# Optimization experiments

Measured on AMD Instinct MI355X. Metric: run time of the kernel, lower is better.

Reference implementation:

```python
import jax, jax.numpy as jnp
import numpy as np

B, T, C = 4, 2048, 1024
H, D, CS = 16, 64, 16   # heads, head dim, titans chunk size
EPS = 1e-5


def setup_inputs():
    key = jax.random.key(0)
    ks = jax.random.split(key, 4)
    s = 0.02
    return {
        "x": jax.random.normal(ks[0], (B, T, C), jnp.float32),
        "W_attn": jax.random.normal(ks[1], (C, 3 * C), jnp.float32) * s,
        "b_attn": jnp.zeros((3 * C,), jnp.float32),
        "W_param": jax.random.normal(ks[2], (C, 3 * H), jnp.float32) * s,
        "b_param": jnp.zeros((3 * H,), jnp.float32),
        "W_proj": jax.random.normal(ks[3], (C, C), jnp.float32) * s,
        "b_proj": jnp.zeros((C,), jnp.float32),
        "w": jnp.ones((H, D), jnp.float32),
        "b": jnp.zeros((H, D), jnp.float32),
    }


def _ln(x, w, b):
    # per-head layernorm over last dim
    mu = x.mean(-1, keepdims=True)
    xc = x - mu
    rstd = jax.lax.rsqrt((xc * xc).mean(-1, keepdims=True) + EPS)
    return xc * rstd * w + b


def _ln_bwd(x, w, dy):
    # gradient of layernorm(x; w, b) w.r.t. x, given upstream dy
    mu = x.mean(-1, keepdims=True)
    xc = x - mu
    rstd = jax.lax.rsqrt((xc * xc).mean(-1, keepdims=True) + EPS)
    xhat = xc * rstd
    wdy = dy * w
    c1 = (xhat * wdy).mean(-1, keepdims=True)
    c2 = wdy.mean(-1, keepdims=True)
    return (wdy - xhat * c1 - c2) * rstd


def _chunk_titans_linear(q, k, v, w, b, theta, alpha, eta):
    # q,k,v: [B,H,T,D]; theta/alpha/eta: [B,H,T,1]; w,b: [H,D]
    NT = T // CS
    wr = w.reshape(1, H, 1, D)
    br = b.reshape(1, H, 1, D)

    def to_chunks(t):
        return t.reshape(B, H, NT, CS, t.shape[-1]).transpose(2, 0, 1, 3, 4)

    qc, kc, vc = to_chunks(q), to_chunks(k), to_chunks(v)
    tc, ac, ec = to_chunks(theta), to_chunks(alpha), to_chunks(eta)

    def chunk_step(carry, inp):
        S, m = carry  # memory state / momentum: [B,H,D,D]
        q_i, k_i, v_i, th_i, al_i, et_i = inp
        # gradients of ||LN(k S) - v||^2 w.r.t. S, taken at the chunk-start state
        kh = jnp.einsum('bhcd,bhde->bhce', k_i, S)
        d_recon = 2.0 * (_ln(kh, wr, br) - v_i)
        dkh = _ln_bwd(kh, wr, d_recon)
        grads = jnp.einsum('bhci,bhcj->bhcij', k_i, dkh)  # [B,H,CS,D,D]

        def tok_step(c2, t_inp):
            S_t, m_t = c2
            g, th, al, et = t_inp
            th = th[..., None]; al = al[..., None]; et = et[..., None]
            m_t = et * m_t - th * g          # momentum
            S_t = (1.0 - al) * S_t + m_t     # weight-decayed state update
            return (S_t, m_t), S_t

        (S, m), S_seq = jax.lax.scan(
            tok_step, (S, m),
            (grads.transpose(2, 0, 1, 3, 4),
             th_i.transpose(2, 0, 1, 3),
             al_i.transpose(2, 0, 1, 3),
             et_i.transpose(2, 0, 1, 3)))
        # read memory with the freshly updated per-token state
        o_i = jnp.einsum('bhcd,cbhde->bhce', q_i, S_seq)
        return (S, m), o_i

    S0 = jnp.zeros((B, H, D, D), q.dtype)
    m0 = jnp.zeros((B, H, D, D), q.dtype)
    _, o_chunks = jax.lax.scan(chunk_step, (S0, m0), (qc, kc, vc, tc, ac, ec))
    o = o_chunks.transpose(1, 2, 0, 3, 4).reshape(B, H, T, D)
    return _ln(o, wr, br)  # normalized memory readout


def reference(x, W_attn, b_attn, W_param, b_param, W_proj, b_proj, w, b):
    qkv = x @ W_attn + b_attn
    q, k, v = jnp.split(qkv, 3, axis=-1)

    def heads(t):
        return t.reshape(B, T, H, D).transpose(0, 2, 1, 3)

    q, k, v = heads(q), heads(k), heads(v)
    q = q / jnp.maximum(jnp.linalg.norm(q, axis=-1, keepdims=True), 1e-12)
    k = k / jnp.maximum(jnp.linalg.norm(k, axis=-1, keepdims=True), 1e-12)
    p = jax.nn.sigmoid((x @ W_param + b_param).reshape(B, T, H, 3).transpose(0, 2, 1, 3))
    theta, alpha, eta = p[..., 0:1], p[..., 1:2], p[..., 2:3]
    o = _chunk_titans_linear(q, k, v, w, b, theta, alpha, eta)
    o = o.transpose(0, 2, 1, 3).reshape(B, T, C)
    return o @ W_proj + b_proj
```

## Files before the change

kernel.cpp:

```cpp
#include <hip/hip_runtime.h>
#include <cstddef>
#include <cstdint>
#include <math.h>

#define BB   4
#define TT   2048
#define CCH  1024
#define HH   16
#define DD   64
#define CSZ  16
#define NTC  128
#define EPSF 1e-5f
#define WVS  8
#define STR  3072

typedef __attribute__((ext_vector_type(8))) short bf16x8;
typedef __attribute__((ext_vector_type(4))) float f32x4;
typedef __attribute__((ext_vector_type(2))) float f32x2;

__device__ __forceinline__ void bar_lds() {
  asm volatile("s_waitcnt lgkmcnt(0)" ::: "memory");
  __builtin_amdgcn_s_barrier();
}

__device__ __forceinline__ uint32_t pack_split(float f) {
  uint32_t b = __float_as_uint(f);
  uint32_t uh = (b + 0x7fffu + ((b >> 16) & 1u)) >> 16;
  float fh = __uint_as_float(uh << 16);
  float r = f - fh;
  return uh | (__float_as_uint(r) & 0xffff0000u);
}
__device__ __forceinline__ float unpack_f(uint32_t u) {
  return __uint_as_float(u << 16) + __uint_as_float(u & 0xffff0000u);
}

__device__ __forceinline__ float wave_sum(float x) {
  float v = x;
  v += __int_as_float(__builtin_amdgcn_update_dpp(0, __float_as_int(v), 0x111, 0xf, 0xf, true));
  v += __int_as_float(__builtin_amdgcn_update_dpp(0, __float_as_int(v), 0x112, 0xf, 0xf, true));
  v += __int_as_float(__builtin_amdgcn_update_dpp(0, __float_as_int(v), 0x114, 0xf, 0xf, true));
  v += __int_as_float(__builtin_amdgcn_update_dpp(0, __float_as_int(v), 0x118, 0xf, 0xf, true));
  v += __int_as_float(__builtin_amdgcn_update_dpp(0, __float_as_int(v), 0x142, 0xa, 0xf, true));
  v += __int_as_float(__builtin_amdgcn_update_dpp(0, __float_as_int(v), 0x143, 0xc, 0xf, true));
  return __int_as_float(__builtin_amdgcn_readlane(__float_as_int(v), 63));
}

__device__ __forceinline__ float red16(float x) {
  float v = x;
  v += __int_as_float(__builtin_amdgcn_update_dpp(0, __float_as_int(v), 0x0B1, 0xf, 0xf, true));
  v += __int_as_float(__builtin_amdgcn_update_dpp(0, __float_as_int(v), 0x04E, 0xf, 0xf, true));
  v += __int_as_float(__builtin_amdgcn_update_dpp(0, __float_as_int(v), 0x124, 0xf, 0xf, true));
  v += __int_as_float(__builtin_amdgcn_update_dpp(0, __float_as_int(v), 0x128, 0xf, 0xf, true));
  return v;
}

__device__ __forceinline__ float sigmoidf_(float x) {
  return 1.f / (1.f + expf(-x));
}

__global__ __launch_bounds__(256) void split_transpose_pl(
    const float* __restrict__ W, unsigned short* __restrict__ Whi,
    unsigned short* __restrict__ Wlo, int K, int N, int rowOff) {
  __shared__ float t[32][33];
  const int n0 = blockIdx.x * 32, k0 = blockIdx.y * 32;
  const int tx = threadIdx.x & 31, ty = threadIdx.x >> 5;
#pragma unroll
  for (int i = 0; i < 4; i++) {
    int n = n0 + tx;
    t[ty + i * 8][tx] = (n < N) ? W[(size_t)(k0 + ty + i * 8) * N + n] : 0.f;
  }
  __syncthreads();
#pragma unroll
  for (int i = 0; i < 4; i++) {
    int n = n0 + ty + i * 8;
    if (n < N) {
      uint32_t ps = pack_split(t[tx][ty + i * 8]);
      size_t off = (size_t)(rowOff + n) * K + k0 + tx;
      Whi[off] = (unsigned short)(ps & 0xffffu);
      Wlo[off] = (unsigned short)(ps >> 16);
    }
  }
}

template<bool A_PACKED, bool C_PACKED, bool NORM>
__global__ __launch_bounds__(256) void gemm_split(
    const void* __restrict__ Av, int lda,
    const unsigned short* __restrict__ Bhg,
    const unsigned short* __restrict__ Blg,
    const float* __restrict__ bias,
    void* __restrict__ Cv, float* __restrict__ Pbuf,
    int M, int ldc, int K, int Nb, int Ns, int pc0) {
  __shared__ unsigned short Ahi[128][40];
  __shared__ unsigned short Alo[128][40];
  __shared__ unsigned short Bhi[128][40];
  __shared__ unsigned short Blo[128][40];

  const int tid = threadIdx.x;
  const int row0 = blockIdx.y * 128;
  const int col0 = blockIdx.x * 128;
  const int wv = tid >> 6;
  const int l  = tid & 63;
  const int wr = wv >> 1, wc = wv & 1;
  const int lrow = l & 15;
  const int kgrp = (l >> 4) * 8;

  const int sr = tid >> 1;
  const int sk = (tid & 1) * 16;

  f32x4 acc[4][4];
#pragma unroll
  for (int i = 0; i < 4; i++)
#pragma unroll
    for (int j = 0; j < 4; j++) acc[i][j] = (f32x4){0.f, 0.f, 0.f, 0.f};

  uint4 pa[4];
  float4 pf[4];
  uint4 pbh[2], pbl[2];

  auto load_tile = [&](int k0) {
    if (A_PACKED) {
      const uint32_t* Ap = (const uint32_t*)Av + (size_t)(row0 + sr) * lda + k0 + sk;
#pragma unroll
      for (int i = 0; i < 4; i++) pa[i] = *(const uint4*)(Ap + i * 4);
    } else {
      const float* Ap = (const float*)Av + (size_t)(row0 + sr) * lda + k0 + sk;
#pragma unroll
      for (int i = 0; i < 4; i++) pf[i] = *(const float4*)(Ap + i * 4);
    }
    if (col0 + sr < Nb) {
      const unsigned short* bh = Bhg + (size_t)(col0 + sr) * K + k0 + sk;
      const unsigned short* bl = Blg + (size_t)(col0 + sr) * K + k0 + sk;
      pbh[0] = *(const uint4*)bh;  pbh[1] = *(const uint4*)(bh + 8);
      pbl[0] = *(const uint4*)bl;  pbl[1] = *(const uint4*)(bl + 8);
    } else {
      pbh[0] = pbh[1] = pbl[0] = pbl[1] = make_uint4(0u, 0u, 0u, 0u);
    }
  };

  auto commit_tile = [&]() {
    uint32_t hp[8], lp[8];
    if (A_PACKED) {
      uint32_t u[16];
#pragma unroll
      for (int i = 0; i < 4; i++) *(uint4*)&u[i * 4] = pa[i];
#pragma unroll
      for (int j = 0; j < 8; j++) {
        hp[j] = (u[2 * j] & 0xffffu) | (u[2 * j + 1] << 16);
        lp[j] = (u[2 * j] >> 16) | (u[2 * j + 1] & 0xffff0000u);
      }
    } else {
      float f[16];
#pragma unroll
      for (int i = 0; i < 4; i++) *(float4*)&f[i * 4] = pf[i];
      uint32_t uh[16], ulr[16];
#pragma unroll
      for (int j = 0; j < 16; j++) {
        uint32_t b = __float_as_uint(f[j]);
        uint32_t h = (b + 0x7fffu + ((b >> 16) & 1u)) >> 16;
        uh[j] = h;
        ulr[j] = __float_as_uint(f[j] - __uint_as_float(h << 16));
      }
#pragma unroll
      for (int j = 0; j < 8; j++) {
        hp[j] = uh[2 * j] | (uh[2 * j + 1] << 16);
        lp[j] = (ulr[2 * j] >> 16) | (ulr[2 * j + 1] & 0xffff0000u);
      }
    }
    *(uint4*)&Ahi[sr][sk]     = *(uint4*)&hp[0];
    *(uint4*)&Ahi[sr][sk + 8] = *(uint4*)&hp[4];
    *(uint4*)&Alo[sr][sk]     = *(uint4*)&lp[0];
    *(uint4*)&Alo[sr][sk + 8] = *(uint4*)&lp[4];
    *(uint4*)&Bhi[sr][sk]     = pbh[0];
    *(uint4*)&Bhi[sr][sk + 8] = pbh[1];
    *(uint4*)&Blo[sr][sk]     = pbl[0];
    *(uint4*)&Blo[sr][sk + 8] = pbl[1];
  };

  load_tile(0);
  for (int k0 = 0; k0 < K; k0 += 32) {
    commit_tile();
    bar_lds();
    if (k0 + 32 < K) load_tile(k0 + 32);

    bf16x8 bh[4], bl[4];
#pragma unroll
    for (int j = 0; j < 4; j++) {
      bh[j] = *(const bf16x8*)&Bhi[wc * 64 + j * 16 + lrow][kgrp];
      bl[j] = *(const bf16x8*)&Blo[wc * 64 + j * 16 + lrow][kgrp];
    }
#pragma unroll
    for (int i = 0; i < 4; i++) {
      bf16x8 ah = *(const bf16x8*)&Ahi[wr * 64 + i * 16 + lrow][kgrp];
      bf16x8 al = *(const bf16x8*)&Alo[wr * 64 + i * 16 + lrow][kgrp];
#pragma unroll
      for (int j = 0; j < 4; j++) {
        acc[i][j] = __builtin_amdgcn_mfma_f32_16x16x32_bf16(ah, bh[j], acc[i][j], 0, 0, 0);
        acc[i][j] = __builtin_amdgcn_mfma_f32_16x16x32_bf16(ah, bl[j], acc[i][j], 0, 0, 0);
        acc[i][j] = __builtin_amdgcn_mfma_f32_16x16x32_bf16(al, bh[j], acc[i][j], 0, 0, 0);
      }
    }
    bar_lds();
  }

  const int crow4 = (l >> 4) * 4;
  if (NORM && col0 < 2048) {
    float bj[4];
#pragma unroll
    for (int j = 0; j < 4; j++) bj[j] = bias[col0 + wc * 64 + j * 16 + lrow];
#pragma unroll
    for (int i = 0; i < 4; i++) {
#pragma unroll
      for (int r = 0; r < 4; r++) {
        float vals[4];
        float ss = 0.f;
#pragma unroll
        for (int j = 0; j < 4; j++) {
          vals[j] = acc[i][j][r] + bj[j];
          ss += vals[j] * vals[j];
        }
        ss = red16(ss);
        float sc = 1.f / fmaxf(sqrtf(ss), 1e-12f);
        const int rowb = row0 + wr * 64 + i * 16 + crow4 + r;
#pragma unroll
        for (int j = 0; j < 4; j++) {
          const int col = col0 + wc * 64 + j * 16 + lrow;
          ((uint32_t*)Cv)[(size_t)rowb * ldc + col] = pack_split(vals[j] * sc);
        }
      }
    }
  } else {
#pragma unroll
    for (int i = 0; i < 4; i++) {
#pragma unroll
      for (int j = 0; j < 4; j++) {
        const int col = col0 + wc * 64 + j * 16 + lrow;
        const float bv = (col < Ns) ? bias[col] : 0.f;
        const int rowb = row0 + wr * 64 + i * 16 + crow4;
#pragma unroll
        for (int r = 0; r < 4; r++) {
          float v = acc[i][j][r] + bv;
          if (col < Ns) {
            if (col >= pc0) {
              Pbuf[(size_t)(rowb + r) * 48 + (col - pc0)] = v;
            } else if (C_PACKED) {
              ((uint32_t*)Cv)[(size_t)(rowb + r) * ldc + col] = pack_split(v);
            } else {
              ((float*)Cv)[(size_t)(rowb + r) * ldc + col] = v;
            }
          }
        }
      }
    }
  }
}

__global__ __launch_bounds__(512) void titans_rec(
    uint32_t* __restrict__ qkv, const float* __restrict__ p,
    const float* __restrict__ w, const float* __restrict__ bparm) {
  const int bh = blockIdx.x;
  const int b = bh >> 4;
  const int h = bh & 15;
  const int tid = threadIdx.x;
  const int wv = tid >> 6;
  const int l = tid & 63;

  __shared__ float k_s[2][CSZ][DD];
  __shared__ float q_s[2][CSZ][DD];
  __shared__ float v_s[CSZ][DD];
  __shared__ float dkh_s[CSZ][DD];
  __shared__ float part[2][WVS][CSZ][DD];
  __shared__ float4 prm_s[2][CSZ];

  f32x2 S2[4], M2[4];
#pragma unroll
  for (int r = 0; r < 4; r++) { S2[r] = (f32x2){0.f, 0.f}; M2[r] = (f32x2){0.f, 0.f}; }

  const float w_l = w[h * DD + l];
  const float b_l = bparm[h * DD + l];

  uint32_t* qbase = qkv + (size_t)(b * TT) * STR + h * DD;
  const float* pbase = p + (size_t)(b * TT) * 48 + h * 3;

  uint32_t rq[2], rk[2], rv[2];
  float rp0 = 0.f, rp1 = 0.f, rp2 = 0.f;
  {
#pragma unroll
    for (int i = 0; i < 2; i++) {
      const int row = wv + i * 8;
      size_t roff = (size_t)row * STR + l;
      q_s[0][row][l] = unpack_f(qbase[roff]);
      k_s[0][row][l] = unpack_f(qbase[roff + 1024]);
      v_s[row][l]    = unpack_f(qbase[roff + 2048]);
    }
    if (tid < CSZ) {
      const float* pp = pbase + (size_t)tid * 48;
      prm_s[0][tid] = make_float4(sigmoidf_(pp[0]), sigmoidf_(pp[1]), sigmoidf_(pp[2]), 0.f);
    }
#pragma unroll
    for (int i = 0; i < 2; i++) {
      size_t roff = (size_t)(CSZ + wv + i * 8) * STR + l;
      rq[i] = qbase[roff];
      rk[i] = qbase[roff + 1024];
      rv[i] = qbase[roff + 2048];
    }
    if (tid < CSZ) {
      const float* pp = pbase + (size_t)(CSZ + tid) * 48;
      rp0 = pp[0]; rp1 = pp[1]; rp2 = pp[2];
    }
  }
  bar_lds();

  for (int nt = 0; nt < NTC; nt++) {
    const int buf = nt & 1;
    float (*partw)[CSZ][DD] = part[buf];
    float (*partr)[CSZ][DD] = part[buf ^ 1];

    if (nt > 0) {
#pragma unroll
      for (int i = 0; i < 2; i++) {
        const int t = wv + i * 8;
        float o = 0.f;
#pragma unroll
        for (int ww = 0; ww < WVS; ww++) o += partr[ww][t][l];
        float mu = wave_sum(o) * (1.f / 64.f);
        float xc = o - mu;
        float var = wave_sum(xc * xc) * (1.f / 64.f);
        float rstd = rsqrtf(var + EPSF);
        float y = xc * rstd * w_l + b_l;
        qbase[(size_t)((nt - 1) * CSZ + t) * STR + 2048 + l] = pack_split(y);
      }
    }
#pragma unroll
    for (int c = 0; c < CSZ; c++) {
      const f32x2* kp2 = (const f32x2*)&k_s[buf][c][wv * 8];
      f32x2 a2;
      a2 = kp2[0] * S2[0];
      a2 = kp2[1] * S2[1] + a2;
      a2 = kp2[2] * S2[2] + a2;
      a2 = kp2[3] * S2[3] + a2;
      partw[wv][c][l] = a2.x + a2.y;
    }
    bar_lds();

#pragma unroll
    for (int i = 0; i < 2; i++) {
      const int c = wv + i * 8;
      float kh = 0.f;
#pragma unroll
      for (int ww = 0; ww < WVS; ww++) kh += partw[ww][c][l];
      float mu = wave_sum(kh) * (1.f / 64.f);
      float xc = kh - mu;
      float var = wave_sum(xc * xc) * (1.f / 64.f);
      float rstd = rsqrtf(var + EPSF);
      float xhat = xc * rstd;
      float y = xhat * w_l + b_l;
      float dy = 2.f * (y - v_s[c][l]);
      float wdy = dy * w_l;
      float c1 = wave_sum(xhat * wdy) * (1.f / 64.f);
      float c2 = wave_sum(wdy) * (1.f / 64.f);
      dkh_s[c][l] = (wdy - xhat * c1 - c2) * rstd;
    }
    bar_lds();

    if (nt + 1 < NTC) {
#pragma unroll
      for (int i = 0; i < 2; i++) {
        const int row = wv + i * 8;
        k_s[buf ^ 1][row][l] = unpack_f(rk[i]);
        q_s[buf ^ 1][row][l] = unpack_f(rq[i]);
        v_s[row][l] = unpack_f(rv[i]);
      }
      if (tid < CSZ)
        prm_s[buf ^ 1][tid] = make_float4(sigmoidf_(rp0), sigmoidf_(rp1), sigmoidf_(rp2), 0.f);
    }
    if (nt + 2 < NTC) {
#pragma unroll
      for (int i = 0; i < 2; i++) {
        size_t roff = (size_t)((nt + 2) * CSZ + wv + i * 8) * STR + l;
        rq[i] = qbase[roff];
        rk[i] = qbase[roff + 1024];
        rv[i] = qbase[roff + 2048];
      }
      if (tid < CSZ) {
        const float* pp = pbase + (size_t)((nt + 2) * CSZ + tid) * 48;
        rp0 = pp[0]; rp1 = pp[1]; rp2 = pp[2];
      }
    }
#pragma unroll
    for (int t = 0; t < CSZ; t++) {
      float4 prm = prm_s[buf][t];
      float a = prm.x * dkh_s[t][l];
      const f32x2 na2 = (f32x2){-a, -a};
      const f32x2 et2 = (f32x2){prm.z, prm.z};
      const f32x2 be2 = (f32x2){1.f - prm.y, 1.f - prm.y};
      const f32x2* kp2 = (const f32x2*)&k_s[buf][t][wv * 8];
      const f32x2* qp2 = (const f32x2*)&q_s[buf][t][wv * 8];
      f32x2 po2 = (f32x2){0.f, 0.f};
#pragma unroll
      for (int pq = 0; pq < 4; pq++) {
        M2[pq] = et2 * M2[pq] + na2 * kp2[pq];
        S2[pq] = be2 * S2[pq] + M2[pq];
        po2    = qp2[pq] * S2[pq] + po2;
      }
      partw[wv][t][l] = po2.x + po2.y;
    }
    bar_lds();
  }

  {
    float (*partr)[CSZ][DD] = part[(NTC - 1) & 1];
#pragma unroll
    for (int i = 0; i < 2; i++) {
      const int t = wv + i * 8;
      float o = 0.f;
#pragma unroll
      for (int ww = 0; ww < WVS; ww++) o += partr[ww][t][l];
      float mu = wave_sum(o) * (1.f / 64.f);
      float xc = o - mu;
      float var = wave_sum(xc * xc) * (1.f / 64.f);
      float rstd = rsqrtf(var + EPSF);
      float y = xc * rstd * w_l + b_l;
      qbase[(size_t)((NTC - 1) * CSZ + t) * STR + 2048 + l] = pack_split(y);
    }
  }
}

extern "C" void kernel_launch(void* const* d_in, const int* in_sizes, int n_in,
                              void* d_out, int out_size, void* d_ws, size_t ws_size,
                              hipStream_t stream) {
  const float* x      = (const float*)d_in[0];
  const float* W_attn = (const float*)d_in[1];
  const float* b_attn = (const float*)d_in[2];
  const float* W_parm = (const float*)d_in[3];
  const float* b_parm = (const float*)d_in[4];
  const float* W_proj = (const float*)d_in[5];
  const float* b_proj = (const float*)d_in[6];
  const float* w      = (const float*)d_in[7];
  const float* bb     = (const float*)d_in[8];
  float* out = (float*)d_out;

  const int M = BB * TT;
  uint32_t* qkv = (uint32_t*)d_ws;
  float* pbf = (float*)(qkv + (size_t)M * STR);
  unsigned short* wattn_hi = (unsigned short*)(pbf + (size_t)M * 48);
  unsigned short* wattn_lo = wattn_hi + (size_t)3120 * 1024;
  unsigned short* wproj_hi = wattn_lo + (size_t)3120 * 1024;
  unsigned short* wproj_lo = wproj_hi + (size_t)1024 * 1024;
  float* bcat = (float*)(wproj_lo + (size_t)1024 * 1024);

  hipMemcpyAsync(bcat, b_attn, 3072 * sizeof(float), hipMemcpyDeviceToDevice, stream);
  hipMemcpyAsync(bcat + 3072, b_parm, 48 * sizeof(float), hipMemcpyDeviceToDevice, stream);

  split_transpose_pl<<<dim3(3072 / 32, 1024 / 32), 256, 0, stream>>>(W_attn, wattn_hi, wattn_lo, 1024, 3072, 0);
  split_transpose_pl<<<dim3(2, 1024 / 32), 256, 0, stream>>>(W_parm, wattn_hi, wattn_lo, 1024, 48, 3072);
  split_transpose_pl<<<dim3(1024 / 32, 1024 / 32), 256, 0, stream>>>(W_proj, wproj_hi, wproj_lo, 1024, 1024, 0);

  gemm_split<false, true, true><<<dim3(25, M / 128), 256, 0, stream>>>(
      x, CCH, wattn_hi, wattn_lo, bcat, qkv, pbf, M, STR, CCH,
      3120, 3120, 3072);
  titans_rec<<<BB * HH, 512, 0, stream>>>(qkv, pbf, w, bb);
  gemm_split<true, false, false><<<dim3(CCH / 128, M / 128), 256, 0, stream>>>(
      qkv + 2048, STR, wproj_hi, wproj_lo, b_proj, out, nullptr, M, CCH, CCH,
      1024, 1024, 1 << 30);
}
```

Before: 903.0 us.

## Pre-split A operands into separate bf16 hi/lo planes for GEMMs

Adds a pre-pass kernel that splits x into separate bf16 hi and lo arrays. The recurrence kernel now writes its normalized output as separate hi/lo planes into the same buffer, which it can reuse once the first GEMM has consumed x. Both GEMMs then load A tiles as ready-made hi/lo bf16 rows and copy them straight into LDS, removing the per-tile split and unpack arithmetic. The cost is an extra launch and an extra read and write pass over x, which adds memory traffic.

```diff
diff --git a/kernel.cpp b/kernel.cpp
--- a/kernel.cpp
+++ b/kernel.cpp
@@ -58,6 +58,23 @@
   return 1.f / (1.f + expf(-x));
 }
 
+__global__ __launch_bounds__(256) void presplit_x(
+    const float* __restrict__ x, unsigned short* __restrict__ xhi,
+    unsigned short* __restrict__ xlo, int n4) {
+  const int i = blockIdx.x * 256 + threadIdx.x;
+  if (i >= n4) return;
+  float4 f = *(const float4*)(x + (size_t)i * 4);
+  uint32_t p0 = pack_split(f.x), p1 = pack_split(f.y);
+  uint32_t p2 = pack_split(f.z), p3 = pack_split(f.w);
+  ushort4 h, lo;
+  h.x = (unsigned short)(p0 & 0xffffu);  lo.x = (unsigned short)(p0 >> 16);
+  h.y = (unsigned short)(p1 & 0xffffu);  lo.y = (unsigned short)(p1 >> 16);
+  h.z = (unsigned short)(p2 & 0xffffu);  lo.z = (unsigned short)(p2 >> 16);
+  h.w = (unsigned short)(p3 & 0xffffu);  lo.w = (unsigned short)(p3 >> 16);
+  *(ushort4*)(xhi + (size_t)i * 4) = h;
+  *(ushort4*)(xlo + (size_t)i * 4) = lo;
+}
+
 __global__ __launch_bounds__(256) void split_transpose_pl(
     const float* __restrict__ W, unsigned short* __restrict__ Whi,
     unsigned short* __restrict__ Wlo, int K, int N, int rowOff) {
@@ -82,9 +99,10 @@
   }
 }
 
-template<bool A_PACKED, bool C_PACKED, bool NORM>
+template<bool C_PACKED, bool NORM>
 __global__ __launch_bounds__(256) void gemm_split(
-    const void* __restrict__ Av, int lda,
+    const unsigned short* __restrict__ Ahg,
+    const unsigned short* __restrict__ Alg, int lda,
     const unsigned short* __restrict__ Bhg,
     const unsigned short* __restrict__ Blg,
     const float* __restrict__ bias,
@@ -113,20 +131,14 @@
 #pragma unroll
     for (int j = 0; j < 4; j++) acc[i][j] = (f32x4){0.f, 0.f, 0.f, 0.f};
 
-  uint4 pa[4];
-  float4 pf[4];
+  uint4 pah[2], pal[2];
   uint4 pbh[2], pbl[2];
 
   auto load_tile = [&](int k0) {
-    if (A_PACKED) {
-      const uint32_t* Ap = (const uint32_t*)Av + (size_t)(row0 + sr) * lda + k0 + sk;
-#pragma unroll
-      for (int i = 0; i < 4; i++) pa[i] = *(const uint4*)(Ap + i * 4);
-    } else {
-      const float* Ap = (const float*)Av + (size_t)(row0 + sr) * lda + k0 + sk;
-#pragma unroll
-      for (int i = 0; i < 4; i++) pf[i] = *(const float4*)(Ap + i * 4);
-    }
+    const unsigned short* ah = Ahg + (size_t)(row0 + sr) * lda + k0 + sk;
+    const unsigned short* al = Alg + (size_t)(row0 + sr) * lda + k0 + sk;
+    pah[0] = *(const uint4*)ah;  pah[1] = *(const uint4*)(ah + 8);
+    pal[0] = *(const uint4*)al;  pal[1] = *(const uint4*)(al + 8);
     if (col0 + sr < Nb) {
       const unsigned short* bh = Bhg + (size_t)(col0 + sr) * K + k0 + sk;
       const unsigned short* bl = Blg + (size_t)(col0 + sr) * K + k0 + sk;
@@ -138,38 +150,10 @@
   };
 
   auto commit_tile = [&]() {
-    uint32_t hp[8], lp[8];
-    if (A_PACKED) {
-      uint32_t u[16];
-#pragma unroll
-      for (int i = 0; i < 4; i++) *(uint4*)&u[i * 4] = pa[i];
-#pragma unroll
-      for (int j = 0; j < 8; j++) {
-        hp[j] = (u[2 * j] & 0xffffu) | (u[2 * j + 1] << 16);
-        lp[j] = (u[2 * j] >> 16) | (u[2 * j + 1] & 0xffff0000u);
-      }
-    } else {
-      float f[16];
-#pragma unroll
-      for (int i = 0; i < 4; i++) *(float4*)&f[i * 4] = pf[i];
-      uint32_t uh[16], ulr[16];
-#pragma unroll
-      for (int j = 0; j < 16; j++) {
-        uint32_t b = __float_as_uint(f[j]);
-        uint32_t h = (b + 0x7fffu + ((b >> 16) & 1u)) >> 16;
-        uh[j] = h;
-        ulr[j] = __float_as_uint(f[j] - __uint_as_float(h << 16));
-      }
-#pragma unroll
-      for (int j = 0; j < 8; j++) {
-        hp[j] = uh[2 * j] | (uh[2 * j + 1] << 16);
-        lp[j] = (ulr[2 * j] >> 16) | (ulr[2 * j + 1] & 0xffff0000u);
-      }
-    }
-    *(uint4*)&Ahi[sr][sk]     = *(uint4*)&hp[0];
-    *(uint4*)&Ahi[sr][sk + 8] = *(uint4*)&hp[4];
-    *(uint4*)&Alo[sr][sk]     = *(uint4*)&lp[0];
-    *(uint4*)&Alo[sr][sk + 8] = *(uint4*)&lp[4];
+    *(uint4*)&Ahi[sr][sk]     = pah[0];
+    *(uint4*)&Ahi[sr][sk + 8] = pah[1];
+    *(uint4*)&Alo[sr][sk]     = pal[0];
+    *(uint4*)&Alo[sr][sk + 8] = pal[1];
     *(uint4*)&Bhi[sr][sk]     = pbh[0];
     *(uint4*)&Bhi[sr][sk + 8] = pbh[1];
     *(uint4*)&Blo[sr][sk]     = pbl[0];
@@ -255,7 +239,8 @@
 }
 
 __global__ __launch_bounds__(512) void titans_rec(
-    uint32_t* __restrict__ qkv, const float* __restrict__ p,
+    const uint32_t* __restrict__ qkv, const float* __restrict__ p,
+    unsigned short* __restrict__ ohi, unsigned short* __restrict__ olo,
     const float* __restrict__ w, const float* __restrict__ bparm) {
   const int bh = blockIdx.x;
   const int b = bh >> 4;
@@ -278,8 +263,10 @@
   const float w_l = w[h * DD + l];
   const float b_l = bparm[h * DD + l];
 
-  uint32_t* qbase = qkv + (size_t)(b * TT) * STR + h * DD;
+  const uint32_t* qbase = qkv + (size_t)(b * TT) * STR + h * DD;
   const float* pbase = p + (size_t)(b * TT) * 48 + h * 3;
+  unsigned short* ohbase = ohi + (size_t)(b * TT) * CCH + h * DD;
+  unsigned short* olbase = olo + (size_t)(b * TT) * CCH + h * DD;
 
   uint32_t rq[2], rk[2], rv[2];
   float rp0 = 0.f, rp1 = 0.f, rp2 = 0.f;
@@ -327,7 +314,10 @@
         float var = wave_sum(xc * xc) * (1.f / 64.f);
         float rstd = rsqrtf(var + EPSF);
         float y = xc * rstd * w_l + b_l;
-        qbase[(size_t)((nt - 1) * CSZ + t) * STR + 2048 + l] = pack_split(y);
+        uint32_t ps = pack_split(y);
+        size_t ooff = (size_t)((nt - 1) * CSZ + t) * CCH + l;
+        ohbase[ooff] = (unsigned short)(ps & 0xffffu);
+        olbase[ooff] = (unsigned short)(ps >> 16);
       }
     }
 #pragma unroll
@@ -420,7 +410,10 @@
       float var = wave_sum(xc * xc) * (1.f / 64.f);
       float rstd = rsqrtf(var + EPSF);
       float y = xc * rstd * w_l + b_l;
-      qbase[(size_t)((NTC - 1) * CSZ + t) * STR + 2048 + l] = pack_split(y);
+      uint32_t ps = pack_split(y);
+      size_t ooff = (size_t)((NTC - 1) * CSZ + t) * CCH + l;
+      ohbase[ooff] = (unsigned short)(ps & 0xffffu);
+      olbase[ooff] = (unsigned short)(ps >> 16);
     }
   }
 }
@@ -442,7 +435,9 @@
   const int M = BB * TT;
   uint32_t* qkv = (uint32_t*)d_ws;
   float* pbf = (float*)(qkv + (size_t)M * STR);
-  unsigned short* wattn_hi = (unsigned short*)(pbf + (size_t)M * 48);
+  unsigned short* xop_hi = (unsigned short*)(pbf + (size_t)M * 48);
+  unsigned short* xop_lo = xop_hi + (size_t)M * CCH;
+  unsigned short* wattn_hi = xop_lo + (size_t)M * CCH;
   unsigned short* wattn_lo = wattn_hi + (size_t)3120 * 1024;
   unsigned short* wproj_hi = wattn_lo + (size_t)3120 * 1024;
   unsigned short* wproj_lo = wproj_hi + (size_t)1024 * 1024;
@@ -451,15 +446,16 @@
   hipMemcpyAsync(bcat, b_attn, 3072 * sizeof(float), hipMemcpyDeviceToDevice, stream);
   hipMemcpyAsync(bcat + 3072, b_parm, 48 * sizeof(float), hipMemcpyDeviceToDevice, stream);
 
+  presplit_x<<<(M * CCH / 4 + 255) / 256, 256, 0, stream>>>(x, xop_hi, xop_lo, M * CCH / 4);
   split_transpose_pl<<<dim3(3072 / 32, 1024 / 32), 256, 0, stream>>>(W_attn, wattn_hi, wattn_lo, 1024, 3072, 0);
   split_transpose_pl<<<dim3(2, 1024 / 32), 256, 0, stream>>>(W_parm, wattn_hi, wattn_lo, 1024, 48, 3072);
   split_transpose_pl<<<dim3(1024 / 32, 1024 / 32), 256, 0, stream>>>(W_proj, wproj_hi, wproj_lo, 1024, 1024, 0);
 
-  gemm_split<false, true, true><<<dim3(25, M / 128), 256, 0, stream>>>(
-      x, CCH, wattn_hi, wattn_lo, bcat, qkv, pbf, M, STR, CCH,
+  gemm_split<true, true><<<dim3(25, M / 128), 256, 0, stream>>>(
+      xop_hi, xop_lo, CCH, wattn_hi, wattn_lo, bcat, qkv, pbf, M, STR, CCH,
       3120, 3120, 3072);
-  titans_rec<<<BB * HH, 512, 0, stream>>>(qkv, pbf, w, bb);
-  gemm_split<true, false, false><<<dim3(CCH / 128, M / 128), 256, 0, stream>>>(
-      qkv + 2048, STR, wproj_hi, wproj_lo, b_proj, out, nullptr, M, CCH, CCH,
+  titans_rec<<<BB * HH, 512, 0, stream>>>(qkv, pbf, xop_hi, xop_lo, w, bb);
+  gemm_split<false, false><<<dim3(CCH / 128, M / 128), 256, 0, stream>>>(
+      xop_hi, xop_lo, CCH, wproj_hi, wproj_lo, b_proj, out, nullptr, M, CCH, CCH,
       1024, 1024, 1 << 30);
 }
```

After: 1.201 ms. +33.1%, slower.

## Restructure titans recurrence loop to compute next-chunk kh alongside token updates

Applied to the files above, without the earlier changes.

Reorders the per-chunk loop so that, right after the token-wise state updates, each wave computes the k·S partial products for the next chunk. It then runs the output layernorm and the next chunk's gradient layernorm in the same phase, which cuts the barriers per chunk from three to two. The first chunk's gradient is computed analytically from the zero state, and v and the prefetch depth gain an extra buffer stage. This costs extra LDS (a second partial buffer and a double-buffered v) and makes chunk ordering more intricate.

```diff
diff --git a/kernel.cpp b/kernel.cpp
--- a/kernel.cpp
+++ b/kernel.cpp
@@ -266,9 +266,10 @@
 
   __shared__ float k_s[2][CSZ][DD];
   __shared__ float q_s[2][CSZ][DD];
-  __shared__ float v_s[CSZ][DD];
+  __shared__ float v_s[2][CSZ][DD];
   __shared__ float dkh_s[CSZ][DD];
-  __shared__ float part[2][WVS][CSZ][DD];
+  __shared__ float partP[WVS][CSZ][DD];
+  __shared__ float partK[WVS][CSZ][DD];
   __shared__ float4 prm_s[2][CSZ];
 
   f32x2 S2[4], M2[4];
@@ -283,109 +284,52 @@
 
   uint32_t rq[2], rk[2], rv[2];
   float rp0 = 0.f, rp1 = 0.f, rp2 = 0.f;
+
   {
 #pragma unroll
+    for (int cc = 0; cc < 2; cc++) {
+#pragma unroll
+      for (int i = 0; i < 2; i++) {
+        const int row = wv + i * 8;
+        size_t roff = (size_t)(cc * CSZ + row) * STR + l;
+        q_s[cc][row][l] = unpack_f(qbase[roff]);
+        k_s[cc][row][l] = unpack_f(qbase[roff + 1024]);
+        v_s[cc][row][l] = unpack_f(qbase[roff + 2048]);
+      }
+      if (tid < CSZ) {
+        const float* pp = pbase + (size_t)(cc * CSZ + tid) * 48;
+        prm_s[cc][tid] = make_float4(sigmoidf_(pp[0]), sigmoidf_(pp[1]), sigmoidf_(pp[2]), 0.f);
+      }
+    }
+#pragma unroll
     for (int i = 0; i < 2; i++) {
-      const int row = wv + i * 8;
-      size_t roff = (size_t)row * STR + l;
-      q_s[0][row][l] = unpack_f(qbase[roff]);
-      k_s[0][row][l] = unpack_f(qbase[roff + 1024]);
-      v_s[row][l]    = unpack_f(qbase[roff + 2048]);
-    }
-    if (tid < CSZ) {
-      const float* pp = pbase + (size_t)tid * 48;
-      prm_s[0][tid] = make_float4(sigmoidf_(pp[0]), sigmoidf_(pp[1]), sigmoidf_(pp[2]), 0.f);
-    }
-#pragma unroll
-    for (int i = 0; i < 2; i++) {
-      size_t roff = (size_t)(CSZ + wv + i * 8) * STR + l;
+      size_t roff = (size_t)(2 * CSZ + wv + i * 8) * STR + l;
       rq[i] = qbase[roff];
       rk[i] = qbase[roff + 1024];
       rv[i] = qbase[roff + 2048];
     }
     if (tid < CSZ) {
-      const float* pp = pbase + (size_t)(CSZ + tid) * 48;
+      const float* pp = pbase + (size_t)(2 * CSZ + tid) * 48;
       rp0 = pp[0]; rp1 = pp[1]; rp2 = pp[2];
+    }
+  }
+  bar_lds();
+  {
+    const float rstd0 = rsqrtf(EPSF);
+#pragma unroll
+    for (int i = 0; i < 2; i++) {
+      const int c = wv + i * 8;
+      float dy = 2.f * (b_l - v_s[0][c][l]);
+      float wdy = dy * w_l;
+      float c2 = wave_sum(wdy) * (1.f / 64.f);
+      dkh_s[c][l] = (wdy - c2) * rstd0;
     }
   }
   bar_lds();
 
   for (int nt = 0; nt < NTC; nt++) {
     const int buf = nt & 1;
-    float (*partw)[CSZ][DD] = part[buf];
-    float (*partr)[CSZ][DD] = part[buf ^ 1];
-
-    if (nt > 0) {
-#pragma unroll
-      for (int i = 0; i < 2; i++) {
-        const int t = wv + i * 8;
-        float o = 0.f;
-#pragma unroll
-        for (int ww = 0; ww < WVS; ww++) o += partr[ww][t][l];
-        float mu = wave_sum(o) * (1.f / 64.f);
-        float xc = o - mu;
-        float var = wave_sum(xc * xc) * (1.f / 64.f);
-        float rstd = rsqrtf(var + EPSF);
-        float y = xc * rstd * w_l + b_l;
-        qbase[(size_t)((nt - 1) * CSZ + t) * STR + 2048 + l] = pack_split(y);
-      }
-    }
-#pragma unroll
-    for (int c = 0; c < CSZ; c++) {
-      const f32x2* kp2 = (const f32x2*)&k_s[buf][c][wv * 8];
-      f32x2 a2;
-      a2 = kp2[0] * S2[0];
-      a2 = kp2[1] * S2[1] + a2;
-      a2 = kp2[2] * S2[2] + a2;
-      a2 = kp2[3] * S2[3] + a2;
-      partw[wv][c][l] = a2.x + a2.y;
-    }
-    bar_lds();
-
-#pragma unroll
-    for (int i = 0; i < 2; i++) {
-      const int c = wv + i * 8;
-      float kh = 0.f;
-#pragma unroll
-      for (int ww = 0; ww < WVS; ww++) kh += partw[ww][c][l];
-      float mu = wave_sum(kh) * (1.f / 64.f);
-      float xc = kh - mu;
-      float var = wave_sum(xc * xc) * (1.f / 64.f);
-      float rstd = rsqrtf(var + EPSF);
-      float xhat = xc * rstd;
-      float y = xhat * w_l + b_l;
-      float dy = 2.f * (y - v_s[c][l]);
-      float wdy = dy * w_l;
-      float c1 = wave_sum(xhat * wdy) * (1.f / 64.f);
-      float c2 = wave_sum(wdy) * (1.f / 64.f);
-      dkh_s[c][l] = (wdy - xhat * c1 - c2) * rstd;
-    }
-    bar_lds();
-
-    if (nt + 1 < NTC) {
-#pragma unroll
-      for (int i = 0; i < 2; i++) {
-        const int row = wv + i * 8;
-        k_s[buf ^ 1][row][l] = unpack_f(rk[i]);
-        q_s[buf ^ 1][row][l] = unpack_f(rq[i]);
-        v_s[row][l] = unpack_f(rv[i]);
-      }
-      if (tid < CSZ)
-        prm_s[buf ^ 1][tid] = make_float4(sigmoidf_(rp0), sigmoidf_(rp1), sigmoidf_(rp2), 0.f);
-    }
-    if (nt + 2 < NTC) {
-#pragma unroll
-      for (int i = 0; i < 2; i++) {
-        size_t roff = (size_t)((nt + 2) * CSZ + wv + i * 8) * STR + l;
-        rq[i] = qbase[roff];
-        rk[i] = qbase[roff + 1024];
-        rv[i] = qbase[roff + 2048];
-      }
-      if (tid < CSZ) {
-        const float* pp = pbase + (size_t)((nt + 2) * CSZ + tid) * 48;
-        rp0 = pp[0]; rp1 = pp[1]; rp2 = pp[2];
-      }
-    }
+
 #pragma unroll
     for (int t = 0; t < CSZ; t++) {
       float4 prm = prm_s[buf][t];
@@ -402,26 +346,80 @@
         S2[pq] = be2 * S2[pq] + M2[pq];
         po2    = qp2[pq] * S2[pq] + po2;
       }
-      partw[wv][t][l] = po2.x + po2.y;
+      partP[wv][t][l] = po2.x + po2.y;
+    }
+    if (nt + 1 < NTC) {
+#pragma unroll
+      for (int c = 0; c < CSZ; c++) {
+        const f32x2* kp2 = (const f32x2*)&k_s[buf ^ 1][c][wv * 8];
+        f32x2 a2;
+        a2 = kp2[0] * S2[0];
+        a2 = kp2[1] * S2[1] + a2;
+        a2 = kp2[2] * S2[2] + a2;
+        a2 = kp2[3] * S2[3] + a2;
+        partK[wv][c][l] = a2.x + a2.y;
+      }
     }
     bar_lds();
-  }
-
-  {
-    float (*partr)[CSZ][DD] = part[(NTC - 1) & 1];
+
 #pragma unroll
     for (int i = 0; i < 2; i++) {
       const int t = wv + i * 8;
       float o = 0.f;
 #pragma unroll
-      for (int ww = 0; ww < WVS; ww++) o += partr[ww][t][l];
+      for (int ww = 0; ww < WVS; ww++) o += partP[ww][t][l];
       float mu = wave_sum(o) * (1.f / 64.f);
       float xc = o - mu;
       float var = wave_sum(xc * xc) * (1.f / 64.f);
       float rstd = rsqrtf(var + EPSF);
       float y = xc * rstd * w_l + b_l;
-      qbase[(size_t)((NTC - 1) * CSZ + t) * STR + 2048 + l] = pack_split(y);
-    }
+      qbase[(size_t)(nt * CSZ + t) * STR + 2048 + l] = pack_split(y);
+    }
+    if (nt + 1 < NTC) {
+#pragma unroll
+      for (int i = 0; i < 2; i++) {
+        const int c = wv + i * 8;
+        float kh = 0.f;
+#pragma unroll
+        for (int ww = 0; ww < WVS; ww++) kh += partK[ww][c][l];
+        float mu = wave_sum(kh) * (1.f / 64.f);
+        float xc = kh - mu;
+        float var = wave_sum(xc * xc) * (1.f / 64.f);
+        float rstd = rsqrtf(var + EPSF);
+        float xhat = xc * rstd;
+        float y = xhat * w_l + b_l;
+        float dy = 2.f * (y - v_s[buf ^ 1][c][l]);
+        float wdy = dy * w_l;
+        float c1 = wave_sum(xhat * wdy) * (1.f / 64.f);
+        float c2 = wave_sum(wdy) * (1.f / 64.f);
+        dkh_s[c][l] = (wdy - xhat * c1 - c2) * rstd;
+      }
+    }
+    if (nt + 2 < NTC) {
+#pragma unroll
+      for (int i = 0; i < 2; i++) {
+        const int row = wv + i * 8;
+        k_s[buf][row][l] = unpack_f(rk[i]);
+        q_s[buf][row][l] = unpack_f(rq[i]);
+        v_s[buf][row][l] = unpack_f(rv[i]);
+      }
+      if (tid < CSZ)
+        prm_s[buf][tid] = make_float4(sigmoidf_(rp0), sigmoidf_(rp1), sigmoidf_(rp2), 0.f);
+    }
+    if (nt + 3 < NTC) {
+#pragma unroll
+      for (int i = 0; i < 2; i++) {
+        size_t roff = (size_t)((nt + 3) * CSZ + wv + i * 8) * STR + l;
+        rq[i] = qbase[roff];
+        rk[i] = qbase[roff + 1024];
+        rv[i] = qbase[roff + 2048];
+      }
+      if (tid < CSZ) {
+        const float* pp = pbase + (size_t)((nt + 3) * CSZ + tid) * 48;
+        rp0 = pp[0]; rp1 = pp[1]; rp2 = pp[2];
+      }
+    }
+    bar_lds();
   }
 }
 
```

Measured after the change: 908.7 us. No clear change (+0.6%).
